# Optimization experiments

Measured on AMD Instinct MI355X. Metric: run time of the kernel, lower is better.

The kernel has to match this reference:

```python
import jax, jax.numpy as jnp
import numpy as np

SCALING = 32.0 / 16.0  # alpha / r


def setup_inputs() -> dict:
    key = jax.random.key(0)
    ks = jax.random.split(key, 6)
    B, S, IN, OUT, R = 4, 2048, 4096, 4096, 16
    x = jax.random.normal(ks[0], (B, S, IN), dtype=jnp.float32)
    # packed 4-bit weights: each int holds two nibbles (values 0..255)
    qweight = jax.random.randint(ks[1], (OUT, IN // 2), 0, 256, dtype=jnp.int32)
    scales = (jax.random.uniform(ks[2], (OUT,), dtype=jnp.float32) * 0.01 + 1e-4).astype(jnp.float16)
    zeros = (jax.random.normal(ks[3], (OUT,), dtype=jnp.float32) * 0.05).astype(jnp.float16)
    lora_A = jax.random.normal(ks[4], (R, IN), dtype=jnp.float32) * (1.0 / np.sqrt(IN))
    lora_B = jax.random.normal(ks[5], (OUT, R), dtype=jnp.float32) * 0.01
    return {"x": x, "qweight": qweight, "scales": scales, "zeros": zeros,
            "lora_A": lora_A, "lora_B": lora_B}


def _dequantize(qweight, scales, zeros):
    # qweight: [O, I//2] packed bytes -> high nibble goes to even cols, low to odd
    high = (qweight >> 4).astype(jnp.float32)          # [O, I//2]
    low = (qweight & 15).astype(jnp.float32)           # [O, I//2]
    O, half = qweight.shape
    w = jnp.stack([high, low], axis=-1).reshape(O, half * 2)  # interleave -> [O, I]
    return w * scales.astype(jnp.float32)[:, None] + zeros.astype(jnp.float32)[:, None]


def reference(x, qweight, scales, zeros, lora_A, lora_B):
    W = _dequantize(qweight, scales, zeros)            # [O, I] fp32
    base = jnp.einsum('bsi,oi->bso', x, W)             # F.linear, no bias
    lora = jnp.einsum('bsi,ri->bsr', x, lora_A)        # [B,S,r]
    lora = jnp.einsum('bsr,or->bso', lora, lora_B) * SCALING
    return base + lora
```

## Files before the change

kernel.cpp:

```cpp
#include <hip/hip_runtime.h>
#include <hip/hip_fp16.h>

#define MDIM 8192
#define NDIM 4096
#define KDIM 4096

typedef unsigned short u16;
typedef __bf16 bf16x8 __attribute__((ext_vector_type(8)));
typedef float f32x4 __attribute__((ext_vector_type(4)));

static __device__ __forceinline__ u16 f2bf(float f) {
  union { float f; unsigned u; } v; v.f = f;
  unsigned r = v.u + 0x7fffu + ((v.u >> 16) & 1u);
  return (u16)(r >> 16);
}

static __device__ __forceinline__ bool sz_is_f32(const void* sc) {
  unsigned w0 = ((const unsigned*)sc)[0];
  return ((w0 >> 16) & 0x7fffu) >= 0x3000u;
}
static __device__ __forceinline__ float load_sz(const void* p, int i, bool f32) {
  return f32 ? ((const float*)p)[i] : __half2float(((const __half*)p)[i]);
}

#define CONVB 2048
#define WEFFB 512
__global__ void qlora_prep(const float4* __restrict__ x, ushort4* __restrict__ xb,
                           const int* __restrict__ qw, const void* __restrict__ sc,
                           const void* __restrict__ zr, const float* __restrict__ lA,
                           const float* __restrict__ lB, ushort2* __restrict__ weff) {
  if (blockIdx.x < CONVB) {
    unsigned base = blockIdx.x * 256u + threadIdx.x;
#pragma unroll
    for (int s = 0; s < 16; ++s) {
      unsigned i = base + (unsigned)s * (CONVB * 256u);
      float4 a = x[i];
      ushort4 o;
      o.x = f2bf(a.x); o.y = f2bf(a.y); o.z = f2bf(a.z); o.w = f2bf(a.w);
      xb[i] = o;
    }
  } else {
    __shared__ __align__(16) float lA_s[16][512];
    __shared__ float lB_s[64][16];
    __shared__ float s_s[64], z_s[64];
    const int bid = blockIdx.x - CONVB;
    const int t = threadIdx.x;
    const int o0 = (bid & 63) * 64;
    const int it0 = (bid >> 6) * 512;
    const bool f32 = sz_is_f32(sc);
#pragma unroll
    for (int s = 0; s < 8; ++s) {
      int idx = s * 256 + t;
      int r = idx >> 7, c4 = idx & 127;
      *(float4*)&lA_s[r][c4 * 4] = *(const float4*)(lA + (size_t)r * KDIM + it0 + c4 * 4);
    }
#pragma unroll
    for (int s = 0; s < 4; ++s) {
      int idx = s * 256 + t;
      int o = idx >> 4, r = idx & 15;
      lB_s[o][r] = lB[(o0 + o) * 16 + r] * 2.0f;
    }
    if (t < 64) {
      s_s[t] = load_sz(sc, o0 + t, f32);
      z_s[t] = load_sz(zr, o0 + t, f32);
    }
    __syncthreads();
    float2 a2[16];
#pragma unroll
    for (int r = 0; r < 16; ++r) a2[r] = *(const float2*)&lA_s[r][2 * t];
    const size_t i2 = (size_t)(it0 / 2 + t);
    const int* qcol = qw + i2;
    ushort2* wcol = weff + i2;
#pragma unroll 4
    for (int o = 0; o < 64; ++o) {
      const int oo = o0 + o;
      int q = qcol[(size_t)oo * (KDIM / 2)];
      float acc0 = 0.f, acc1 = 0.f;
#pragma unroll
      for (int r = 0; r < 16; ++r) {
        float br = lB_s[o][r];
        acc0 += br * a2[r].x;
        acc1 += br * a2[r].y;
      }
      const float s = s_s[o], z = z_s[o];
      float w0 = (float)((q >> 4) & 15) * s + z + acc0;
      float w1 = (float)(q & 15) * s + z + acc1;
      ushort2 pk; pk.x = f2bf(w0); pk.y = f2bf(w1);
      wcol[(size_t)oo * (KDIM / 2)] = pk;
    }
  }
}


#define STAGE(SB, BUFSEL, REGOFF, HALF, KT) do {                                   \
    const u16* _s0 = (SB) + (size_t)(HALF) * (128 * (size_t)KDIM) + (KT) * 64;     \
    u16* _d0 = lds + (BUFSEL) * 32768 + (REGOFF) + (HALF) * 8192 + wave * 1024;    \
    __builtin_amdgcn_global_load_lds(                                              \
        (const __attribute__((address_space(1))) void*)_s0,                        \
        (__attribute__((address_space(3))) void*)_d0, 16, 0, 0);                   \
    __builtin_amdgcn_global_load_lds(                                              \
        (const __attribute__((address_space(1))) void*)(_s0 + 8 * KDIM),           \
        (__attribute__((address_space(3))) void*)(_d0 + 512), 16, 0, 0);           \
  } while (0)

#define SBAR0 __builtin_amdgcn_sched_barrier(0)

__global__ __launch_bounds__(512, 2) void qlora_gemm_p(const u16* __restrict__ A,
                                                       const u16* __restrict__ B,
                                                       float* __restrict__ C) {
  __shared__ __align__(16) u16 lds[65536];

  const int t = threadIdx.x;
  const int lane = t & 63;
  const int wave = t >> 6;
  const int wr = wave >> 2;
  const int wc = wave & 3;
  const int lrow = lane & 15;
  const int khalf = lane >> 4;
  const int g0 = (khalf ^ (lane & 7)) * 8;

  const int flat = blockIdx.x;
  const int xcd = flat & 7;
  const int idx = flat >> 3;
  const int brow = ((xcd & 3) * 8 + (idx & 7)) * 256;
  const int bcol = ((xcd >> 2) * 8 + (idx >> 3)) * 256;

  const int aRowBase = (wr * 64 + lrow) * 64 + g0;
  const int bRowBase = 16384 + (wc * 64 + lrow) * 64 + g0;

  const int srow = wave * 16 + (lane >> 3);
  const int sg = ((lane & 7) ^ ((lane >> 3) & 7)) * 8;
  const u16* aS = A + (size_t)(brow + srow) * KDIM + sg;
  const u16* bS = B + (size_t)(bcol + srow) * KDIM + sg;

  f32x4 acc[2][4][4] = {};

  STAGE(aS, 0, 0, 0, 0);
  STAGE(bS, 0, 16384, 0, 0);
  STAGE(bS, 0, 16384, 1, 0);
  STAGE(aS, 0, 0, 1, 0);

#pragma unroll 1
  for (int it = 0; it < KDIM / 64; ++it) {
    const int buf = it & 1;
    const int nbuf = buf ^ 1;
    const int nxt = (it + 1) & 63;
    const int abase = buf * 32768;

    asm volatile("s_waitcnt vmcnt(2)" ::: "memory");
    SBAR0;
    __builtin_amdgcn_s_barrier();
    SBAR0;

    bf16x8 af0[4], af1[4], bfr0[4], bfr1[4];
#pragma unroll
    for (int mf = 0; mf < 4; ++mf)
      af0[mf] = *(const bf16x8*)(lds + (abase + aRowBase + mf * 1024));
#pragma unroll
    for (int nf = 0; nf < 4; ++nf)
      bfr0[nf] = *(const bf16x8*)(lds + (abase + bRowBase + nf * 1024));
#pragma unroll
    for (int mf = 0; mf < 4; ++mf)
      af1[mf] = *(const bf16x8*)(lds + ((abase + aRowBase + mf * 1024) ^ 32));
#pragma unroll
    for (int nf = 0; nf < 4; ++nf)
      bfr1[nf] = *(const bf16x8*)(lds + ((abase + bRowBase + nf * 1024) ^ 32));
    SBAR0;
    STAGE(aS, nbuf, 0, 0, nxt);
    STAGE(bS, nbuf, 16384, 0, nxt);
    SBAR0;

    __builtin_amdgcn_s_setprio(1);
#pragma unroll
    for (int mf = 0; mf < 4; ++mf)
#pragma unroll
      for (int nf = 0; nf < 4; ++nf)
        acc[0][mf][nf] = __builtin_amdgcn_mfma_f32_16x16x32_bf16(af0[mf], bfr0[nf], acc[0][mf][nf], 0, 0, 0);
    __builtin_amdgcn_s_setprio(0);
    SBAR0;
    STAGE(bS, nbuf, 16384, 1, nxt);
    SBAR0;

    asm volatile("s_waitcnt vmcnt(6)" ::: "memory");
    SBAR0;
    __builtin_amdgcn_s_barrier();
    SBAR0;

    bf16x8 af2[4], af3[4];
#pragma unroll
    for (int mf = 0; mf < 4; ++mf)
      af2[mf] = *(const bf16x8*)(lds + (abase + 8192 + aRowBase + mf * 1024));
    SBAR0;

    __builtin_amdgcn_s_setprio(1);
#pragma unroll
    for (int mf = 0; mf < 4; ++mf)
#pragma unroll
      for (int nf = 0; nf < 4; ++nf)
        acc[0][mf][nf] = __builtin_amdgcn_mfma_f32_16x16x32_bf16(af1[mf], bfr1[nf], acc[0][mf][nf], 0, 0, 0);
    __builtin_amdgcn_s_setprio(0);
    SBAR0;

#pragma unroll
    for (int mf = 0; mf < 4; ++mf)
      af3[mf] = *(const bf16x8*)(lds + ((abase + 8192 + aRowBase + mf * 1024) ^ 32));
    STAGE(aS, nbuf, 0, 1, nxt);
    SBAR0;

    __builtin_amdgcn_s_setprio(1);
#pragma unroll
    for (int mf = 0; mf < 4; ++mf)
#pragma unroll
      for (int nf = 0; nf < 4; ++nf)
        acc[1][mf][nf] = __builtin_amdgcn_mfma_f32_16x16x32_bf16(af2[mf], bfr0[nf], acc[1][mf][nf], 0, 0, 0);
    __builtin_amdgcn_s_setprio(0);
    SBAR0;

    __builtin_amdgcn_s_setprio(1);
#pragma unroll
    for (int mf = 0; mf < 4; ++mf)
#pragma unroll
      for (int nf = 0; nf < 4; ++nf)
        acc[1][mf][nf] = __builtin_amdgcn_mfma_f32_16x16x32_bf16(af3[mf], bfr1[nf], acc[1][mf][nf], 0, 0, 0);
    __builtin_amdgcn_s_setprio(0);
    SBAR0;
  }

  asm volatile("s_waitcnt vmcnt(0) lgkmcnt(0)" ::: "memory");

  float* Cb = C + (size_t)brow * NDIM + bcol;
  const int rb = wr * 64 + (lane >> 4) * 4;
  const int cb = wc * 64 + lrow;
#pragma unroll
  for (int qm = 0; qm < 2; ++qm)
#pragma unroll
    for (int mf = 0; mf < 4; ++mf)
#pragma unroll
      for (int nf = 0; nf < 4; ++nf) {
        const int r = qm * 128 + rb + mf * 16;
        const int c = cb + nf * 16;
        f32x4 v = acc[qm][mf][nf];
#pragma unroll
        for (int q = 0; q < 4; ++q)
          Cb[(size_t)(r + q) * NDIM + c] = v[q];
      }
}

__global__ void qlora_fallback(const float* __restrict__ X, const int* __restrict__ qw,
                               const void* __restrict__ sc, const void* __restrict__ zr,
                               const float* __restrict__ lA, const float* __restrict__ lB,
                               float* __restrict__ C) {
  __shared__ float Xs[32][65];
  __shared__ float Ws[32][65];
  const int t = threadIdx.x;
  const bool f32 = sz_is_f32(sc);
  const int brow = blockIdx.x * 64, bcol = blockIdx.y * 64;
  const int tr = t >> 4, tc = t & 15;
  float acc[4][4] = {};
  for (int k0 = 0; k0 < KDIM; k0 += 32) {
    __syncthreads();
    {
      int row = t >> 2;
      int kk0 = (t & 3) * 8;
      const float* src = X + (size_t)(brow + row) * KDIM + k0 + kk0;
#pragma unroll
      for (int u = 0; u < 8; ++u) Xs[kk0 + u][row] = src[u];
    }
    {
      int o = t >> 2;
      int kk0 = (t & 3) * 8;
      int oo = bcol + o;
      float s = load_sz(sc, oo, f32), z = load_sz(zr, oo, f32);
      const int* qrow = qw + (size_t)oo * (KDIM / 2) + (k0 + kk0) / 2;
#pragma unroll
      for (int u = 0; u < 4; ++u) {
        int q = qrow[u];
        int kk = kk0 + u * 2;
        float l0 = 0.f, l1 = 0.f;
#pragma unroll
        for (int r = 0; r < 16; ++r) {
          float br = lB[oo * 16 + r] * 2.0f;
          l0 += br * lA[(size_t)r * KDIM + k0 + kk];
          l1 += br * lA[(size_t)r * KDIM + k0 + kk + 1];
        }
        Ws[kk][o] = (float)((q >> 4) & 15) * s + z + l0;
        Ws[kk + 1][o] = (float)(q & 15) * s + z + l1;
      }
    }
    __syncthreads();
#pragma unroll
    for (int k = 0; k < 32; ++k) {
      float xv[4], wv[4];
#pragma unroll
      for (int i = 0; i < 4; ++i) xv[i] = Xs[k][tr * 4 + i];
#pragma unroll
      for (int j = 0; j < 4; ++j) wv[j] = Ws[k][tc * 4 + j];
#pragma unroll
      for (int i = 0; i < 4; ++i)
#pragma unroll
        for (int j = 0; j < 4; ++j) acc[i][j] += xv[i] * wv[j];
    }
  }
#pragma unroll
  for (int i = 0; i < 4; ++i)
#pragma unroll
    for (int j = 0; j < 4; ++j)
      C[(size_t)(brow + tr * 4 + i) * NDIM + bcol + tc * 4 + j] = acc[i][j];
}

extern "C" void kernel_launch(void* const* d_in, const int* in_sizes, int n_in,
                              void* d_out, int out_size, void* d_ws, size_t ws_size,
                              hipStream_t stream) {
  const float* x = (const float*)d_in[0];
  const int* qw = (const int*)d_in[1];
  const void* sc = d_in[2];
  const void* zr = d_in[3];
  const float* lA = (const float*)d_in[4];
  const float* lB = (const float*)d_in[5];
  float* out = (float*)d_out;

  const size_t xb_bytes = (size_t)MDIM * KDIM * 2;
  const size_t weff_bytes = (size_t)NDIM * KDIM * 2;
  if (ws_size >= xb_bytes + weff_bytes) {
    u16* xb = (u16*)d_ws;
    u16* weff = xb + (size_t)MDIM * KDIM;
    qlora_prep<<<CONVB + WEFFB, 256, 0, stream>>>((const float4*)x, (ushort4*)xb,
                                                  qw, sc, zr, lA, lB, (ushort2*)weff);
    dim3 grid((MDIM / 256) * (NDIM / 256));
    qlora_gemm_p<<<grid, 512, 0, stream>>>(xb, weff, out);
  } else {
    dim3 grid(MDIM / 64, NDIM / 64);
    qlora_fallback<<<grid, 256, 0, stream>>>(x, qw, sc, zr, lA, lB, out);
  }
}
```

Baseline: 293.0 us.

## Restructure GEMM: A operand in registers from global, B via LDS, 32x32 MFMA

Rewrites the main GEMM kernel so each wave loads its A fragments directly from global memory into registers, and only the B tile is staged through a halved, swizzled, double-buffered LDS. It also switches from 16x16x32 to 32x32x16 bf16 MFMA instructions and simplifies the schedule to one barrier per K step. The aim is to cut LDS traffic and footprint and to reduce the number of MFMA issues. In exchange, A is no longer shared between waves through LDS, which raises global/L2 traffic and register pressure. The detailed prio/sched_barrier interleaving is also dropped.

```diff
diff --git a/kernel.cpp b/kernel.cpp
--- a/kernel.cpp
+++ b/kernel.cpp
@@ -8,6 +8,7 @@
 typedef unsigned short u16;
 typedef __bf16 bf16x8 __attribute__((ext_vector_type(8)));
 typedef float f32x4 __attribute__((ext_vector_type(4)));
+typedef float f32x16 __attribute__((ext_vector_type(16)));
 
 static __device__ __forceinline__ u16 f2bf(float f) {
   union { float f; unsigned u; } v; v.f = f;
@@ -92,32 +93,20 @@
 }
 
 
-#define STAGE(SB, BUFSEL, REGOFF, HALF, KT) do {                                   \
-    const u16* _s0 = (SB) + (size_t)(HALF) * (128 * (size_t)KDIM) + (KT) * 64;     \
-    u16* _d0 = lds + (BUFSEL) * 32768 + (REGOFF) + (HALF) * 8192 + wave * 1024;    \
-    __builtin_amdgcn_global_load_lds(                                              \
-        (const __attribute__((address_space(1))) void*)_s0,                        \
-        (__attribute__((address_space(3))) void*)_d0, 16, 0, 0);                   \
-    __builtin_amdgcn_global_load_lds(                                              \
-        (const __attribute__((address_space(1))) void*)(_s0 + 8 * KDIM),           \
-        (__attribute__((address_space(3))) void*)(_d0 + 512), 16, 0, 0);           \
-  } while (0)
-
-#define SBAR0 __builtin_amdgcn_sched_barrier(0)
-
-__global__ __launch_bounds__(512, 2) void qlora_gemm_p(const u16* __restrict__ A,
+__global__ __launch_bounds__(512, 2) void qlora_gemm_g(const u16* __restrict__ A,
                                                        const u16* __restrict__ B,
                                                        float* __restrict__ C) {
-  __shared__ __align__(16) u16 lds[65536];
+  __shared__ __align__(16) u16 lds[32768];
 
   const int t = threadIdx.x;
   const int lane = t & 63;
   const int wave = t >> 6;
   const int wr = wave >> 2;
   const int wc = wave & 3;
-  const int lrow = lane & 15;
-  const int khalf = lane >> 4;
-  const int g0 = (khalf ^ (lane & 7)) * 8;
+  const int l31 = lane & 31;
+  const int l15 = lane & 15;
+  const int l5 = lane >> 5;
+  const int gb = l5 ^ l15;
 
   const int flat = blockIdx.x;
   const int xcd = flat & 7;
@@ -125,125 +114,93 @@
   const int brow = ((xcd & 3) * 8 + (idx & 7)) * 256;
   const int bcol = ((xcd >> 2) * 8 + (idx >> 3)) * 256;
 
-  const int aRowBase = (wr * 64 + lrow) * 64 + g0;
-  const int bRowBase = 16384 + (wc * 64 + lrow) * 64 + g0;
-
-  const int srow = wave * 16 + (lane >> 3);
-  const int sg = ((lane & 7) ^ ((lane >> 3) & 7)) * 8;
-  const u16* aS = A + (size_t)(brow + srow) * KDIM + sg;
-  const u16* bS = B + (size_t)(bcol + srow) * KDIM + sg;
-
-  f32x4 acc[2][4][4] = {};
-
-  STAGE(aS, 0, 0, 0, 0);
-  STAGE(bS, 0, 16384, 0, 0);
-  STAGE(bS, 0, 16384, 1, 0);
-  STAGE(aS, 0, 0, 1, 0);
+  const u16* aP = A + (size_t)(brow + wr * 128 + l31) * KDIM + l5 * 8;
+
+  const u16* bP[4];
+#pragma unroll
+  for (int s = 0; s < 4; ++s) {
+    int g = s * 512 + t;
+    int R = g >> 4;
+    int gS = g & 15;
+    int gL = gS ^ (R & 15);
+    int n = R + ((gL >> 3) << 7);
+    int kb = (gL & 7) * 8;
+    bP[s] = B + (size_t)(bcol + n) * KDIM + kb;
+  }
+
+  f32x16 acc[4][2] = {};
+  bf16x8 a[4][4];
+
+#pragma unroll
+  for (int s = 0; s < 4; ++s)
+    __builtin_amdgcn_global_load_lds(
+        (const __attribute__((address_space(1))) void*)(bP[s]),
+        (__attribute__((address_space(3))) void*)(lds + s * 4096 + wave * 512), 16, 0, 0);
+  __builtin_amdgcn_sched_barrier(0);
+#pragma unroll
+  for (int mf = 0; mf < 4; ++mf)
+#pragma unroll
+    for (int ks = 0; ks < 4; ++ks)
+      a[mf][ks] = *(const bf16x8*)(aP + (size_t)mf * (32 * KDIM) + ks * 16);
 
 #pragma unroll 1
-  for (int it = 0; it < KDIM / 64; ++it) {
+  for (int it = 0; it < 64; ++it) {
     const int buf = it & 1;
-    const int nbuf = buf ^ 1;
-    const int nxt = (it + 1) & 63;
-    const int abase = buf * 32768;
-
-    asm volatile("s_waitcnt vmcnt(2)" ::: "memory");
-    SBAR0;
+    const u16* bbase = lds + buf * 16384;
+
+    asm volatile("s_waitcnt vmcnt(16)" ::: "memory");
     __builtin_amdgcn_s_barrier();
-    SBAR0;
-
-    bf16x8 af0[4], af1[4], bfr0[4], bfr1[4];
-#pragma unroll
-    for (int mf = 0; mf < 4; ++mf)
-      af0[mf] = *(const bf16x8*)(lds + (abase + aRowBase + mf * 1024));
-#pragma unroll
-    for (int nf = 0; nf < 4; ++nf)
-      bfr0[nf] = *(const bf16x8*)(lds + (abase + bRowBase + nf * 1024));
-#pragma unroll
-    for (int mf = 0; mf < 4; ++mf)
-      af1[mf] = *(const bf16x8*)(lds + ((abase + aRowBase + mf * 1024) ^ 32));
-#pragma unroll
-    for (int nf = 0; nf < 4; ++nf)
-      bfr1[nf] = *(const bf16x8*)(lds + ((abase + bRowBase + nf * 1024) ^ 32));
-    SBAR0;
-    STAGE(aS, nbuf, 0, 0, nxt);
-    STAGE(bS, nbuf, 16384, 0, nxt);
-    SBAR0;
-
-    __builtin_amdgcn_s_setprio(1);
-#pragma unroll
-    for (int mf = 0; mf < 4; ++mf)
-#pragma unroll
-      for (int nf = 0; nf < 4; ++nf)
-        acc[0][mf][nf] = __builtin_amdgcn_mfma_f32_16x16x32_bf16(af0[mf], bfr0[nf], acc[0][mf][nf], 0, 0, 0);
-    __builtin_amdgcn_s_setprio(0);
-    SBAR0;
-    STAGE(bS, nbuf, 16384, 1, nxt);
-    SBAR0;
-
-    asm volatile("s_waitcnt vmcnt(6)" ::: "memory");
-    SBAR0;
-    __builtin_amdgcn_s_barrier();
-    SBAR0;
-
-    bf16x8 af2[4], af3[4];
-#pragma unroll
-    for (int mf = 0; mf < 4; ++mf)
-      af2[mf] = *(const bf16x8*)(lds + (abase + 8192 + aRowBase + mf * 1024));
-    SBAR0;
-
-    __builtin_amdgcn_s_setprio(1);
-#pragma unroll
-    for (int mf = 0; mf < 4; ++mf)
-#pragma unroll
-      for (int nf = 0; nf < 4; ++nf)
-        acc[0][mf][nf] = __builtin_amdgcn_mfma_f32_16x16x32_bf16(af1[mf], bfr1[nf], acc[0][mf][nf], 0, 0, 0);
-    __builtin_amdgcn_s_setprio(0);
-    SBAR0;
-
-#pragma unroll
-    for (int mf = 0; mf < 4; ++mf)
-      af3[mf] = *(const bf16x8*)(lds + ((abase + 8192 + aRowBase + mf * 1024) ^ 32));
-    STAGE(aS, nbuf, 0, 1, nxt);
-    SBAR0;
-
-    __builtin_amdgcn_s_setprio(1);
-#pragma unroll
-    for (int mf = 0; mf < 4; ++mf)
-#pragma unroll
-      for (int nf = 0; nf < 4; ++nf)
-        acc[1][mf][nf] = __builtin_amdgcn_mfma_f32_16x16x32_bf16(af2[mf], bfr0[nf], acc[1][mf][nf], 0, 0, 0);
-    __builtin_amdgcn_s_setprio(0);
-    SBAR0;
-
-    __builtin_amdgcn_s_setprio(1);
-#pragma unroll
-    for (int mf = 0; mf < 4; ++mf)
-#pragma unroll
-      for (int nf = 0; nf < 4; ++nf)
-        acc[1][mf][nf] = __builtin_amdgcn_mfma_f32_16x16x32_bf16(af3[mf], bfr1[nf], acc[1][mf][nf], 0, 0, 0);
-    __builtin_amdgcn_s_setprio(0);
-    SBAR0;
+    __builtin_amdgcn_sched_barrier(0);
+
+    if (it != 63) {
+      u16* dst = lds + (buf ^ 1) * 16384 + wave * 512;
+#pragma unroll
+      for (int s = 0; s < 4; ++s)
+        __builtin_amdgcn_global_load_lds(
+            (const __attribute__((address_space(1))) void*)(bP[s] + (it + 1) * 64),
+            (__attribute__((address_space(3))) void*)(dst + s * 4096), 16, 0, 0);
+    }
+    __builtin_amdgcn_sched_barrier(0);
+
+#pragma unroll
+    for (int ks = 0; ks < 4; ++ks) {
+      const int n00 = wc * 64;
+      const int n01 = wc * 64 + 32;
+      bf16x8 b0 = *(const bf16x8*)(bbase + ((n00 & 127) + l31) * 128 +
+                                   ((((n00 >> 7) * 8 + ks * 2) ^ gb) * 8));
+      bf16x8 b1 = *(const bf16x8*)(bbase + ((n01 & 127) + l31) * 128 +
+                                   ((((n01 >> 7) * 8 + ks * 2) ^ gb) * 8));
+#pragma unroll
+      for (int mf = 0; mf < 4; ++mf)
+        acc[mf][0] = __builtin_amdgcn_mfma_f32_32x32x16_bf16(a[mf][ks], b0, acc[mf][0], 0, 0, 0);
+#pragma unroll
+      for (int mf = 0; mf < 4; ++mf)
+        acc[mf][1] = __builtin_amdgcn_mfma_f32_32x32x16_bf16(a[mf][ks], b1, acc[mf][1], 0, 0, 0);
+    }
+
+    if (it != 63) {
+#pragma unroll
+      for (int mf = 0; mf < 4; ++mf)
+#pragma unroll
+        for (int ks = 0; ks < 4; ++ks)
+          a[mf][ks] = *(const bf16x8*)(aP + (size_t)mf * (32 * KDIM) + (it + 1) * 64 + ks * 16);
+    }
   }
 
   asm volatile("s_waitcnt vmcnt(0) lgkmcnt(0)" ::: "memory");
 
-  float* Cb = C + (size_t)brow * NDIM + bcol;
-  const int rb = wr * 64 + (lane >> 4) * 4;
-  const int cb = wc * 64 + lrow;
-#pragma unroll
-  for (int qm = 0; qm < 2; ++qm)
-#pragma unroll
-    for (int mf = 0; mf < 4; ++mf)
-#pragma unroll
-      for (int nf = 0; nf < 4; ++nf) {
-        const int r = qm * 128 + rb + mf * 16;
-        const int c = cb + nf * 16;
-        f32x4 v = acc[qm][mf][nf];
-#pragma unroll
-        for (int q = 0; q < 4; ++q)
-          Cb[(size_t)(r + q) * NDIM + c] = v[q];
+  float* Cb = C + (size_t)(brow + wr * 128) * NDIM + bcol + wc * 64;
+#pragma unroll
+  for (int mf = 0; mf < 4; ++mf)
+#pragma unroll
+    for (int nf = 0; nf < 2; ++nf) {
+      f32x16 v = acc[mf][nf];
+#pragma unroll
+      for (int r = 0; r < 16; ++r) {
+        int row = mf * 32 + (r & 3) + 8 * (r >> 2) + 4 * l5;
+        Cb[(size_t)row * NDIM + nf * 32 + l31] = v[r];
       }
+    }
 }
 
 __global__ void qlora_fallback(const float* __restrict__ X, const int* __restrict__ qw,
@@ -327,7 +284,7 @@
     qlora_prep<<<CONVB + WEFFB, 256, 0, stream>>>((const float4*)x, (ushort4*)xb,
                                                   qw, sc, zr, lA, lB, (ushort2*)weff);
     dim3 grid((MDIM / 256) * (NDIM / 256));
-    qlora_gemm_p<<<grid, 512, 0, stream>>>(xb, weff, out);
+    qlora_gemm_g<<<grid, 512, 0, stream>>>(xb, weff, out);
   } else {
     dim3 grid(MDIM / 64, NDIM / 64);
     qlora_fallback<<<grid, 256, 0, stream>>>(x, qw, sc, zr, lA, lB, out);
```

New measurement: 651.9 us. 2.22x slower.

## Switch GEMM inner loop from 16x16x32 to 32x32x16 bf16 MFMA tiles

Applied to the files above, without the earlier changes.

Replaces the 16x16x32 MFMA fragments with 32x32x16 MFMA instructions. The LDS fragment addressing, the accumulator layout (f32x16) and the output store mapping are all rewritten to match. Each wave now issues fewer, larger MFMAs per K-tile and B fragments are reused across both M halves. This is meant to cut LDS read traffic and instruction issue overhead. In exchange it changes the pipeline interleaving, dropping the separate second-half k phases, and uses a store pattern with 32 lanes per row.

```diff
diff --git a/kernel.cpp b/kernel.cpp
--- a/kernel.cpp
+++ b/kernel.cpp
@@ -8,6 +8,7 @@
 typedef unsigned short u16;
 typedef __bf16 bf16x8 __attribute__((ext_vector_type(8)));
 typedef float f32x4 __attribute__((ext_vector_type(4)));
+typedef float f32x16 __attribute__((ext_vector_type(16)));
 
 static __device__ __forceinline__ u16 f2bf(float f) {
   union { float f; unsigned u; } v; v.f = f;
@@ -105,7 +106,7 @@
 
 #define SBAR0 __builtin_amdgcn_sched_barrier(0)
 
-__global__ __launch_bounds__(512, 2) void qlora_gemm_p(const u16* __restrict__ A,
+__global__ __launch_bounds__(512, 2) void qlora_gemm32(const u16* __restrict__ A,
                                                        const u16* __restrict__ B,
                                                        float* __restrict__ C) {
   __shared__ __align__(16) u16 lds[65536];
@@ -115,9 +116,9 @@
   const int wave = t >> 6;
   const int wr = wave >> 2;
   const int wc = wave & 3;
-  const int lrow = lane & 15;
-  const int khalf = lane >> 4;
-  const int g0 = (khalf ^ (lane & 7)) * 8;
+  const int l31 = lane & 31;
+  const int l5 = lane >> 5;
+  const int gx = l31 & 7;
 
   const int flat = blockIdx.x;
   const int xcd = flat & 7;
@@ -125,15 +126,16 @@
   const int brow = ((xcd & 3) * 8 + (idx & 7)) * 256;
   const int bcol = ((xcd >> 2) * 8 + (idx >> 3)) * 256;
 
-  const int aRowBase = (wr * 64 + lrow) * 64 + g0;
-  const int bRowBase = 16384 + (wc * 64 + lrow) * 64 + g0;
+  const int aBase = (wr * 64 + l31) * 64;
+  const int bBase = 16384 + (wc * 64 + l31) * 64;
 
   const int srow = wave * 16 + (lane >> 3);
   const int sg = ((lane & 7) ^ ((lane >> 3) & 7)) * 8;
   const u16* aS = A + (size_t)(brow + srow) * KDIM + sg;
   const u16* bS = B + (size_t)(bcol + srow) * KDIM + sg;
 
-  f32x4 acc[2][4][4] = {};
+  f32x16 acc0[2][2] = {};
+  f32x16 acc1[2][2] = {};
 
   STAGE(aS, 0, 0, 0, 0);
   STAGE(bS, 0, 16384, 0, 0);
@@ -152,19 +154,19 @@
     __builtin_amdgcn_s_barrier();
     SBAR0;
 
-    bf16x8 af0[4], af1[4], bfr0[4], bfr1[4];
-#pragma unroll
-    for (int mf = 0; mf < 4; ++mf)
-      af0[mf] = *(const bf16x8*)(lds + (abase + aRowBase + mf * 1024));
-#pragma unroll
-    for (int nf = 0; nf < 4; ++nf)
-      bfr0[nf] = *(const bf16x8*)(lds + (abase + bRowBase + nf * 1024));
-#pragma unroll
-    for (int mf = 0; mf < 4; ++mf)
-      af1[mf] = *(const bf16x8*)(lds + ((abase + aRowBase + mf * 1024) ^ 32));
-#pragma unroll
-    for (int nf = 0; nf < 4; ++nf)
-      bfr1[nf] = *(const bf16x8*)(lds + ((abase + bRowBase + nf * 1024) ^ 32));
+    bf16x8 a0[2][4], b0[2][4];
+#pragma unroll
+    for (int mf2 = 0; mf2 < 2; ++mf2)
+#pragma unroll
+      for (int ks = 0; ks < 4; ++ks)
+        a0[mf2][ks] = *(const bf16x8*)(lds + (abase + aBase + mf2 * 2048 +
+                                              (((2 * ks + l5) ^ gx) * 8)));
+#pragma unroll
+    for (int nf2 = 0; nf2 < 2; ++nf2)
+#pragma unroll
+      for (int ks = 0; ks < 4; ++ks)
+        b0[nf2][ks] = *(const bf16x8*)(lds + (abase + bBase + nf2 * 2048 +
+                                              (((2 * ks + l5) ^ gx) * 8)));
     SBAR0;
     STAGE(aS, nbuf, 0, 0, nxt);
     STAGE(bS, nbuf, 16384, 0, nxt);
@@ -172,10 +174,13 @@
 
     __builtin_amdgcn_s_setprio(1);
 #pragma unroll
-    for (int mf = 0; mf < 4; ++mf)
-#pragma unroll
-      for (int nf = 0; nf < 4; ++nf)
-        acc[0][mf][nf] = __builtin_amdgcn_mfma_f32_16x16x32_bf16(af0[mf], bfr0[nf], acc[0][mf][nf], 0, 0, 0);
+    for (int mf2 = 0; mf2 < 2; ++mf2)
+#pragma unroll
+      for (int nf2 = 0; nf2 < 2; ++nf2)
+#pragma unroll
+        for (int ks = 0; ks < 4; ++ks)
+          acc0[mf2][nf2] = __builtin_amdgcn_mfma_f32_32x32x16_bf16(
+              a0[mf2][ks], b0[nf2][ks], acc0[mf2][nf2], 0, 0, 0);
     __builtin_amdgcn_s_setprio(0);
     SBAR0;
     STAGE(bS, nbuf, 16384, 1, nxt);
@@ -186,64 +191,57 @@
     __builtin_amdgcn_s_barrier();
     SBAR0;
 
-    bf16x8 af2[4], af3[4];
-#pragma unroll
-    for (int mf = 0; mf < 4; ++mf)
-      af2[mf] = *(const bf16x8*)(lds + (abase + 8192 + aRowBase + mf * 1024));
+    bf16x8 a1[2][4];
+#pragma unroll
+    for (int mf2 = 0; mf2 < 2; ++mf2)
+#pragma unroll
+      for (int ks = 0; ks < 4; ++ks)
+        a1[mf2][ks] = *(const bf16x8*)(lds + (abase + 8192 + aBase + mf2 * 2048 +
+                                              (((2 * ks + l5) ^ gx) * 8)));
+    STAGE(aS, nbuf, 0, 1, nxt);
     SBAR0;
 
     __builtin_amdgcn_s_setprio(1);
 #pragma unroll
-    for (int mf = 0; mf < 4; ++mf)
-#pragma unroll
-      for (int nf = 0; nf < 4; ++nf)
-        acc[0][mf][nf] = __builtin_amdgcn_mfma_f32_16x16x32_bf16(af1[mf], bfr1[nf], acc[0][mf][nf], 0, 0, 0);
+    for (int mf2 = 0; mf2 < 2; ++mf2)
+#pragma unroll
+      for (int nf2 = 0; nf2 < 2; ++nf2)
+#pragma unroll
+        for (int ks = 0; ks < 4; ++ks)
+          acc1[mf2][nf2] = __builtin_amdgcn_mfma_f32_32x32x16_bf16(
+              a1[mf2][ks], b0[nf2][ks], acc1[mf2][nf2], 0, 0, 0);
     __builtin_amdgcn_s_setprio(0);
     SBAR0;
-
-#pragma unroll
-    for (int mf = 0; mf < 4; ++mf)
-      af3[mf] = *(const bf16x8*)(lds + ((abase + 8192 + aRowBase + mf * 1024) ^ 32));
-    STAGE(aS, nbuf, 0, 1, nxt);
-    SBAR0;
-
-    __builtin_amdgcn_s_setprio(1);
-#pragma unroll
-    for (int mf = 0; mf < 4; ++mf)
-#pragma unroll
-      for (int nf = 0; nf < 4; ++nf)
-        acc[1][mf][nf] = __builtin_amdgcn_mfma_f32_16x16x32_bf16(af2[mf], bfr0[nf], acc[1][mf][nf], 0, 0, 0);
-    __builtin_amdgcn_s_setprio(0);
-    SBAR0;
-
-    __builtin_amdgcn_s_setprio(1);
-#pragma unroll
-    for (int mf = 0; mf < 4; ++mf)
-#pragma unroll
-      for (int nf = 0; nf < 4; ++nf)
-        acc[1][mf][nf] = __builtin_amdgcn_mfma_f32_16x16x32_bf16(af3[mf], bfr1[nf], acc[1][mf][nf], 0, 0, 0);
-    __builtin_amdgcn_s_setprio(0);
-    SBAR0;
   }
 
   asm volatile("s_waitcnt vmcnt(0) lgkmcnt(0)" ::: "memory");
 
   float* Cb = C + (size_t)brow * NDIM + bcol;
-  const int rb = wr * 64 + (lane >> 4) * 4;
-  const int cb = wc * 64 + lrow;
-#pragma unroll
-  for (int qm = 0; qm < 2; ++qm)
-#pragma unroll
-    for (int mf = 0; mf < 4; ++mf)
-#pragma unroll
-      for (int nf = 0; nf < 4; ++nf) {
-        const int r = qm * 128 + rb + mf * 16;
-        const int c = cb + nf * 16;
-        f32x4 v = acc[qm][mf][nf];
-#pragma unroll
-        for (int q = 0; q < 4; ++q)
-          Cb[(size_t)(r + q) * NDIM + c] = v[q];
+#pragma unroll
+  for (int mf2 = 0; mf2 < 2; ++mf2)
+#pragma unroll
+    for (int nf2 = 0; nf2 < 2; ++nf2) {
+      {
+        f32x16 v = acc0[mf2][nf2];
+        const int r0 = wr * 64 + mf2 * 32;
+        const int c0 = wc * 64 + nf2 * 32 + l31;
+#pragma unroll
+        for (int r = 0; r < 16; ++r) {
+          int row = r0 + (r & 3) + 8 * (r >> 2) + 4 * l5;
+          Cb[(size_t)row * NDIM + c0] = v[r];
+        }
       }
+      {
+        f32x16 v = acc1[mf2][nf2];
+        const int r0 = 128 + wr * 64 + mf2 * 32;
+        const int c0 = wc * 64 + nf2 * 32 + l31;
+#pragma unroll
+        for (int r = 0; r < 16; ++r) {
+          int row = r0 + (r & 3) + 8 * (r >> 2) + 4 * l5;
+          Cb[(size_t)row * NDIM + c0] = v[r];
+        }
+      }
+    }
 }
 
 __global__ void qlora_fallback(const float* __restrict__ X, const int* __restrict__ qw,
@@ -327,7 +325,7 @@
     qlora_prep<<<CONVB + WEFFB, 256, 0, stream>>>((const float4*)x, (ushort4*)xb,
                                                   qw, sc, zr, lA, lB, (ushort2*)weff);
     dim3 grid((MDIM / 256) * (NDIM / 256));
-    qlora_gemm_p<<<grid, 512, 0, stream>>>(xb, weff, out);
+    qlora_gemm32<<<grid, 512, 0, stream>>>(xb, weff, out);
   } else {
     dim3 grid(MDIM / 64, NDIM / 64);
     qlora_fallback<<<grid, 256, 0, stream>>>(x, qw, sc, zr, lA, lB, out);
```

Measured after the change: 325.7 us. 11.2% more time.
